# Kernel optimization log

Measured on AMD Instinct MI355X. Metric: run time of the kernel, lower is better.

## Reference

```python
import jax, jax.numpy as jnp
import numpy as np

B, T, E = 4, 2048, 512
H, D = 8, 64            # num_heads, head_size = E // H
HID = H * E             # FFN hidden = num_heads * n_embed (per source)
EPS = 1e-5


def layer_norm(x, g, b):
    mu = jnp.mean(x, axis=-1, keepdims=True)
    var = jnp.var(x, axis=-1, keepdims=True)
    return (x - mu) * jax.lax.rsqrt(var + EPS) * g + b


def setup_inputs() -> dict:
    key = jax.random.key(0)
    ks = jax.random.split(key, 12)
    s_e = 1.0 / np.sqrt(E)
    s_hd = 1.0 / np.sqrt(H * D)
    s_hid = 1.0 / np.sqrt(HID)
    return {
        "x": jax.random.normal(ks[0], (B, T, E), jnp.float32),
        "Wq": jax.random.normal(ks[1], (H, E, D), jnp.float32) * s_e,
        "Wk": jax.random.normal(ks[2], (H, E, D), jnp.float32) * s_e,
        "Wv": jax.random.normal(ks[3], (H, E, D), jnp.float32) * s_e,
        "Wo": jax.random.normal(ks[4], (H * D, E), jnp.float32) * s_hd,
        "bo": jnp.zeros((E,), jnp.float32),
        "W1": jax.random.normal(ks[5], (E, HID), jnp.float32) * s_e,
        "b1": jnp.zeros((HID,), jnp.float32),
        "W2": jax.random.normal(ks[6], (HID, E), jnp.float32) * s_hid,
        "b2": jnp.zeros((E,), jnp.float32),
        "g1": jnp.ones((E,), jnp.float32),
        "be1": jnp.zeros((E,), jnp.float32),
        "g2": jnp.ones((E,), jnp.float32),
        "be2": jnp.zeros((E,), jnp.float32),
    }


def reference(x, Wq, Wk, Wv, Wo, bo, W1, b1, W2, b2, g1, be1, g2, be2):
    # pre-LN decoder block (layer_norm_first=True path)
    xn = layer_norm(x, g1, be1)

    # multi-head causal attention; NOTE: scale is T**-0.5 per the source code
    q = jnp.einsum('bte,hed->bhtd', xn, Wq)
    k = jnp.einsum('bte,hed->bhtd', xn, Wk)
    v = jnp.einsum('bte,hed->bhtd', xn, Wv)
    scores = jnp.einsum('bhtd,bhsd->bhts', q, k) * (T ** -0.5)
    causal = jnp.tril(jnp.ones((T, T), bool))
    scores = jnp.where(causal, scores, -jnp.inf)
    attn = jax.nn.softmax(scores, axis=-1)
    o = jnp.einsum('bhts,bhsd->bhtd', attn, v)           # [B,H,T,D]
    o = o.transpose(0, 2, 1, 3).reshape(B, T, H * D)      # concat heads
    mha = o @ Wo + bo

    x = xn + mha
    xn2 = layer_norm(x, g2, be2)
    ffn = jax.nn.relu(xn2 @ W1 + b1) @ W2 + b2
    return xn2 + ffn
```

## Files before the change

kernel.cpp:

```cpp
#include <hip/hip_runtime.h>
#include <hip/hip_bf16.h>
#include <math.h>

#define Bsz 4
#define Tt 2048
#define Ee 512
#define Hh 8
#define Dd 64
#define HIDs 4096
#define Mrows (Bsz * Tt)

typedef __attribute__((ext_vector_type(8))) short short8;
typedef __attribute__((ext_vector_type(4))) float f32x4;
typedef __attribute__((ext_vector_type(16))) float f32x16;

#define AS1 __attribute__((address_space(1)))
#define AS3 __attribute__((address_space(3)))

__device__ __forceinline__ unsigned short f2bfu(float f) {
    unsigned u = __float_as_uint(f);
    return (unsigned short)((u + 0x7fffu + ((u >> 16) & 1u)) >> 16);
}
__device__ __forceinline__ unsigned short truncbf(float f) {
    return (unsigned short)(__float_as_uint(f) >> 16);
}

__device__ __forceinline__ short8 ld_sw(const __hip_bfloat16* base, int R, int sl) {
    return *(const short8*)(base + R * 32 + (((sl) ^ ((R >> 1) & 3)) << 3));
}

__device__ __forceinline__ void ln_body(const float* __restrict__ x,
        const float* __restrict__ g, const float* __restrict__ b,
        const float* __restrict__ addb,
        float* __restrict__ out_f, __hip_bfloat16* __restrict__ out_bf,
        int row) {
    int tid = threadIdx.x;
    const float* xr = x + (size_t)row * Ee;
    float v0 = xr[tid];
    float v1 = xr[tid + 256];
    float s = v0 + v1;
    float sq = v0 * v0 + v1 * v1;
#pragma unroll
    for (int off = 32; off > 0; off >>= 1) {
        s  += __shfl_xor(s, off, 64);
        sq += __shfl_xor(sq, off, 64);
    }
    __shared__ float ls[4], lq[4];
    int wid = tid >> 6, lane = tid & 63;
    if (lane == 0) { ls[wid] = s; lq[wid] = sq; }
    __syncthreads();
    s  = ls[0] + ls[1] + ls[2] + ls[3];
    sq = lq[0] + lq[1] + lq[2] + lq[3];
    float mean = s * (1.0f / Ee);
    float var  = sq * (1.0f / Ee) - mean * mean;
    float rstd = rsqrtf(var + 1e-5f);
    float o0 = (v0 - mean) * rstd * g[tid]       + b[tid];
    float o1 = (v1 - mean) * rstd * g[tid + 256] + b[tid + 256];
    float* orow = out_f + (size_t)row * Ee;
    orow[tid]       = o0 + addb[tid];
    orow[tid + 256] = o1 + addb[tid + 256];
    __hip_bfloat16* brow = out_bf + (size_t)row * Ee;
    brow[tid]       = __float2bfloat16(o0);
    brow[tid + 256] = __float2bfloat16(o1);
}

__global__ __launch_bounds__(256) void ln_kernel(const float* __restrict__ x,
        const float* __restrict__ g, const float* __restrict__ b,
        const float* __restrict__ addb,
        float* __restrict__ out_f, __hip_bfloat16* __restrict__ out_bf) {
    ln_body(x, g, b, addb, out_f, out_bf, blockIdx.x);
}

__device__ __forceinline__ void tr_tile(const float* __restrict__ in,
        __hip_bfloat16* __restrict__ outp, int R, int C, int c0, int r0) {
    __shared__ float tile[64][65];
    int tc = threadIdx.x & 63, tg = threadIdx.x >> 6;
#pragma unroll
    for (int i = 0; i < 16; ++i) {
        int r = tg * 16 + i;
        tile[r][tc] = in[(size_t)(r0 + r) * C + c0 + tc];
    }
    __syncthreads();
#pragma unroll
    for (int i = 0; i < 16; ++i) {
        int cc = tg * 16 + i;
        outp[(size_t)(c0 + cc) * R + r0 + tc] = __float2bfloat16(tile[tc][cc]);
    }
}
__global__ __launch_bounds__(256) void startup_kernel(
        const float* __restrict__ x, const float* __restrict__ g1,
        const float* __restrict__ be1, const float* __restrict__ bo,
        float* __restrict__ xn, __hip_bfloat16* __restrict__ xn_bf,
        const float* __restrict__ Wq, const float* __restrict__ Wk,
        const float* __restrict__ Wv, const float* __restrict__ Wo,
        const float* __restrict__ W1, const float* __restrict__ W2,
        __hip_bfloat16* __restrict__ bqT, __hip_bfloat16* __restrict__ woT,
        __hip_bfloat16* __restrict__ w1T, __hip_bfloat16* __restrict__ w2T) {
    if (blockIdx.x < Mrows) {
        ln_body(x, g1, be1, bo, xn, xn_bf, blockIdx.x);
        return;
    }
    int blk = blockIdx.x - Mrows;
    if (blk < 192) {
        int p = blk >> 6, h = (blk >> 3) & 7, et = blk & 7;
        const float* W = (p == 0) ? Wq : ((p == 1) ? Wk : Wv);
        float sc = (p == 0) ? 0.022097086912079608f * 1.4426950408889634f : 1.0f;
        __shared__ float tile[64][65];
        int td = threadIdx.x & 63, tg = threadIdx.x >> 6;
#pragma unroll
        for (int i = 0; i < 16; ++i) {
            int e = tg * 16 + i;
            tile[e][td] = W[((size_t)h * Ee + et * 64 + e) * Dd + td] * sc;
        }
        __syncthreads();
#pragma unroll
        for (int i = 0; i < 16; ++i) {
            int d = tg * 16 + i;
            bqT[((size_t)(p * 512 + h * 64 + d)) * Ee + et * 64 + td] =
                __float2bfloat16(tile[td][d]);
        }
    } else if (blk < 256) {
        int t = blk - 192;
        tr_tile(Wo, woT, 512, 512, (t & 7) * 64, (t >> 3) * 64);
    } else if (blk < 768) {
        int t = blk - 256;
        tr_tile(W1, w1T, 512, HIDs, (t & 63) * 64, (t >> 6) * 64);
    } else {
        int t = blk - 768;
        tr_tile(W2, w2T, HIDs, 512, (t & 7) * 64, (t >> 3) * 64);
    }
}

__global__ __launch_bounds__(256) void mfma_gemm(
        const __hip_bfloat16* __restrict__ A, int lda,
        const __hip_bfloat16* __restrict__ B, int ldb,
        __hip_bfloat16* __restrict__ Cb, int ldc, int K, int nx) {
    __shared__ __hip_bfloat16 S[32768];
    int tid = threadIdx.x;
    int lane = tid & 63, wave = tid >> 6;
    int wm = wave >> 1, wn = wave & 1;
    int L = blockIdx.x;
    int slots = (int)gridDim.x >> 3;
    int v = (L & 7) * slots + (L >> 3);
    int bx = v % nx, by = v / nx;
    int row0 = by * 128, col0 = bx * 128;
    f32x4 acc[4][4];
#pragma unroll
    for (int i = 0; i < 4; ++i)
#pragma unroll
        for (int j = 0; j < 4; ++j) acc[i][j] = (f32x4){0.f, 0.f, 0.f, 0.f};

    int fr = lane & 15, sl = lane >> 4;
    int T = K >> 6;

#define STAGEQ(tt, bb)                                                        \
    do {                                                                      \
        int kk_ = (tt) * 64;                                                  \
        _Pragma("unroll")                                                     \
        for (int j = 0; j < 4; ++j) {                                         \
            int c = j * 256 + tid;                                            \
            int p = c >> 9, cp = c & 511;                                     \
            int r = cp >> 2, s = cp & 3;                                      \
            int kg = ((s ^ ((r >> 1) & 3)) << 3);                             \
            int cb = j * 256 + wave * 64;                                     \
            int ko = kk_ + p * 32 + kg;                                       \
            __builtin_amdgcn_global_load_lds(                                 \
                (const AS1 void*)(A + (size_t)(row0 + r) * lda + ko),         \
                (AS3 void*)(S + (bb) * 16384 + cb * 8), 16, 0, 0);            \
            __builtin_amdgcn_global_load_lds(                                 \
                (const AS1 void*)(B + (size_t)(col0 + r) * ldb + ko),         \
                (AS3 void*)(S + (bb) * 16384 + 8192 + cb * 8), 16, 0, 0);     \
        }                                                                     \
    } while (0)

    STAGEQ(0, 0);
    for (int t = 0; t < T; ++t) {
        int tn = (t + 1 < T) ? t + 1 : 0;
        STAGEQ(tn, (t + 1) & 1);
        asm volatile("s_waitcnt vmcnt(8)" ::: "memory");
        __builtin_amdgcn_s_barrier();
        asm volatile("" ::: "memory");
        const __hip_bfloat16* Ab = S + (t & 1) * 16384;
        const __hip_bfloat16* Bb = Ab + 8192;
#pragma unroll
        for (int ks = 0; ks < 2; ++ks) {
            short8 afr[4], bfr[4];
#pragma unroll
            for (int i = 0; i < 4; ++i) {
                afr[i] = ld_sw(Ab + ks * 4096, wm * 64 + i * 16 + fr, sl);
                bfr[i] = ld_sw(Bb + ks * 4096, wn * 64 + i * 16 + fr, sl);
            }
#pragma unroll
            for (int i = 0; i < 4; ++i)
#pragma unroll
                for (int j = 0; j < 4; ++j)
                    acc[i][j] = __builtin_amdgcn_mfma_f32_16x16x32_bf16(afr[i], bfr[j], acc[i][j], 0, 0, 0);
        }
        asm volatile("" ::: "memory");
        __builtin_amdgcn_s_barrier();
        asm volatile("" ::: "memory");
    }
#undef STAGEQ
    asm volatile("s_waitcnt vmcnt(0)" ::: "memory");
    __syncthreads();
    unsigned short* Ew = (unsigned short*)S + wave * 1152;
    const __hip_bfloat16* Er = (const __hip_bfloat16*)Ew;
    int rq = (lane >> 4) << 2;
    int rr = lane >> 2, cb2 = (lane & 3) * 16;
#pragma unroll
    for (int i = 0; i < 4; ++i) {
#pragma unroll
        for (int j = 0; j < 4; ++j)
#pragma unroll
            for (int gi = 0; gi < 4; ++gi)
                Ew[(rq + gi) * 72 + j * 16 + fr] = f2bfu(acc[i][j][gi]);
        uint4 v0 = *(const uint4*)(Er + rr * 72 + cb2);
        uint4 v1 = *(const uint4*)(Er + rr * 72 + cb2 + 8);
        size_t rg = (size_t)(row0 + wm * 64 + i * 16 + rr) * ldc + col0 + wn * 64 + cb2;
        *(uint4*)(Cb + rg)     = v0;
        *(uint4*)(Cb + rg + 8) = v1;
    }
}

__global__ __launch_bounds__(256) void mfma_gemm_n64(
        const __hip_bfloat16* __restrict__ A, int lda,
        const __hip_bfloat16* __restrict__ B, int ldb,
        float* __restrict__ Cf, int ldc, int K, int nx) {
    __shared__ __hip_bfloat16 S[36864];
    int tid = threadIdx.x;
    int lane = tid & 63, wave = tid >> 6;
    int L = blockIdx.x;
    int slots = (int)gridDim.x >> 3;
    int v = (L & 7) * slots + (L >> 3);
    int bx = v % nx, by = v / nx;
    int row0 = by * 128, col0 = bx * 64;
    f32x4 acc[2][4];
#pragma unroll
    for (int i = 0; i < 2; ++i)
#pragma unroll
        for (int j = 0; j < 4; ++j) acc[i][j] = (f32x4){0.f, 0.f, 0.f, 0.f};

    int fr = lane & 15, sl = lane >> 4;
    int T = K >> 6;

#define STAGEN(tt, bb)                                                        \
    do {                                                                      \
        int kk_ = (tt) * 64;                                                  \
        _Pragma("unroll")                                                     \
        for (int j = 0; j < 4; ++j) {                                         \
            int c = j * 256 + tid;                                            \
            int p = c >> 9, cp = c & 511;                                     \
            int r = cp >> 2, s = cp & 3;                                      \
            int kg = ((s ^ ((r >> 1) & 3)) << 3);                             \
            int cb = j * 256 + wave * 64;                                     \
            __builtin_amdgcn_global_load_lds(                                 \
                (const AS1 void*)(A + (size_t)(row0 + r) * lda + kk_ + p * 32 + kg), \
                (AS3 void*)(S + (bb) * 12288 + cb * 8), 16, 0, 0);            \
        }                                                                     \
        _Pragma("unroll")                                                     \
        for (int j = 0; j < 2; ++j) {                                         \
            int c = j * 256 + tid;                                            \
            int p = c >> 8, cp = c & 255;                                     \
            int r = cp >> 2, s = cp & 3;                                      \
            int kg = ((s ^ ((r >> 1) & 3)) << 3);                             \
            int cb = j * 256 + wave * 64;                                     \
            __builtin_amdgcn_global_load_lds(                                 \
                (const AS1 void*)(B + (size_t)(col0 + r) * ldb + kk_ + p * 32 + kg), \
                (AS3 void*)(S + (bb) * 12288 + 8192 + cb * 8), 16, 0, 0);     \
        }                                                                     \
    } while (0)

    STAGEN(0, 0);
    STAGEN(1, 1);
    for (int t = 0; t < T; ++t) {
        int tn = (t + 2 < T) ? t + 2 : 0;
        STAGEN(tn, (t + 2) % 3);
        asm volatile("s_waitcnt vmcnt(12)" ::: "memory");
        __builtin_amdgcn_s_barrier();
        asm volatile("" ::: "memory");
        const __hip_bfloat16* Ab = S + (t % 3) * 12288;
        const __hip_bfloat16* Bb = Ab + 8192;
#pragma unroll
        for (int ks = 0; ks < 2; ++ks) {
            short8 afr[2], bfr[4];
#pragma unroll
            for (int i = 0; i < 2; ++i)
                afr[i] = ld_sw(Ab + ks * 4096, wave * 32 + i * 16 + fr, sl);
#pragma unroll
            for (int j = 0; j < 4; ++j)
                bfr[j] = ld_sw(Bb + ks * 2048, j * 16 + fr, sl);
#pragma unroll
            for (int i = 0; i < 2; ++i)
#pragma unroll
                for (int j = 0; j < 4; ++j)
                    acc[i][j] = __builtin_amdgcn_mfma_f32_16x16x32_bf16(afr[i], bfr[j], acc[i][j], 0, 0, 0);
        }
        asm volatile("" ::: "memory");
        __builtin_amdgcn_s_barrier();
        asm volatile("" ::: "memory");
    }
#undef STAGEN
    asm volatile("s_waitcnt vmcnt(0)" ::: "memory");
    int rq = (lane >> 4) << 2;
#pragma unroll
    for (int i = 0; i < 2; ++i)
#pragma unroll
        for (int j = 0; j < 4; ++j)
#pragma unroll
            for (int gidx = 0; gidx < 4; ++gidx) {
                int r = row0 + wave * 32 + i * 16 + rq + gidx;
                int c = col0 + j * 16 + fr;
                Cf[(size_t)r * ldc + c] += acc[i][j][gidx];
            }
}

__device__ __forceinline__ short8 ld_frag(const __hip_bfloat16* base, int r, int slot) {
    return *(const short8*)(base + r * 64 + ((slot ^ (r & 7)) << 3));
}

__global__ __launch_bounds__(512, 2) void gemm256_8ph(
        const __hip_bfloat16* __restrict__ A, int lda,
        const __hip_bfloat16* __restrict__ B, int ldb,
        __hip_bfloat16* __restrict__ Cb, int ldc, int K,
        const float* __restrict__ bias, int nx) {
    __shared__ __hip_bfloat16 S[65536];
    __hip_bfloat16* Asb = S;
    __hip_bfloat16* Bsb = S + 32768;
    int tid = threadIdx.x;
    int lane = tid & 63, wave = tid >> 6;
    int wm = wave >> 2, wn = wave & 3;
    int fr = lane & 15, l5 = lane >> 4;
    int L = blockIdx.x;
    int slots = (int)gridDim.x >> 3;
    int v = (L & 7) * slots + (L >> 3);
    int bx = v % nx, by = v / nx;
    int row0 = by * 256, col0 = bx * 256;
    int T = K >> 6;

    f32x4 acc[8][4];
#pragma unroll
    for (int i = 0; i < 8; ++i)
#pragma unroll
        for (int j = 0; j < 4; ++j) acc[i][j] = (f32x4){0.f, 0.f, 0.f, 0.f};

#define STAGE_A(tt, hh, bb)                                                   \
    do {                                                                      \
        _Pragma("unroll")                                                     \
        for (int j = 0; j < 2; ++j) {                                         \
            int c = j * 512 + tid;                                            \
            int r = c >> 3;                                                   \
            int sl = (c & 7) ^ (r & 7);                                       \
            int cb = j * 512 + wave * 64;                                     \
            int grow = row0 + ((r >> 6) << 7) + (hh) * 64 + (r & 63);         \
            __builtin_amdgcn_global_load_lds(                                 \
                (const AS1 void*)(A + (size_t)grow * lda + (tt) * 64 + sl * 8), \
                (AS3 void*)(Asb + (bb) * 16384 + (hh) * 8192 + cb * 8), 16, 0, 0); \
        }                                                                     \
    } while (0)
#define STAGE_B(tt, hh, bb)                                                   \
    do {                                                                      \
        _Pragma("unroll")                                                     \
        for (int j = 0; j < 2; ++j) {                                         \
            int c = j * 512 + tid;                                            \
            int r = c >> 3;                                                   \
            int sl = (c & 7) ^ (r & 7);                                       \
            int cb = j * 512 + wave * 64;                                     \
            int gcol = col0 + ((r >> 5) << 6) + (hh) * 32 + (r & 31);         \
            __builtin_amdgcn_global_load_lds(                                 \
                (const AS1 void*)(B + (size_t)gcol * ldb + (tt) * 64 + sl * 8), \
                (AS3 void*)(Bsb + (bb) * 16384 + (hh) * 8192 + cb * 8), 16, 0, 0); \
        }                                                                     \
    } while (0)

    STAGE_A(0, 0, 0);
    STAGE_B(0, 0, 0);
    STAGE_B(0, 1, 0);
    STAGE_A(0, 1, 0);

    short8 a[4][2], b[2][2][2];
    for (int t = 0; t < T; ++t) {
        int buf = t & 1, nb = buf ^ 1;
        int tn = (t + 1 < T) ? t + 1 : 0;
        const __hip_bfloat16* Ab0 = Asb + buf * 16384;
        const __hip_bfloat16* Ab1 = Ab0 + 8192;
        const __hip_bfloat16* Bb0 = Bsb + buf * 16384;
        const __hip_bfloat16* Bb1 = Bb0 + 8192;

        STAGE_A(tn, 0, nb);
        asm volatile("s_waitcnt vmcnt(6)" ::: "memory");
        __builtin_amdgcn_s_barrier();
        asm volatile("" ::: "memory");
#pragma unroll
        for (int i = 0; i < 4; ++i)
#pragma unroll
            for (int ks = 0; ks < 2; ++ks)
                a[i][ks] = ld_frag(Ab0, wm * 64 + i * 16 + fr, ks * 4 + l5);
#pragma unroll
        for (int jj = 0; jj < 2; ++jj)
#pragma unroll
            for (int ks = 0; ks < 2; ++ks)
                b[0][jj][ks] = ld_frag(Bb0, wn * 32 + jj * 16 + fr, ks * 4 + l5);
        __builtin_amdgcn_s_setprio(1);
#pragma unroll
        for (int i = 0; i < 4; ++i)
#pragma unroll
            for (int jj = 0; jj < 2; ++jj)
#pragma unroll
                for (int ks = 0; ks < 2; ++ks)
                    acc[i][jj] = __builtin_amdgcn_mfma_f32_16x16x32_bf16(
                        a[i][ks], b[0][jj][ks], acc[i][jj], 0, 0, 0);
        __builtin_amdgcn_s_setprio(0);
        asm volatile("" ::: "memory");
        __builtin_amdgcn_s_barrier();
        asm volatile("" ::: "memory");

        STAGE_B(tn, 0, nb);
        asm volatile("s_waitcnt vmcnt(6)" ::: "memory");
        __builtin_amdgcn_s_barrier();
        asm volatile("" ::: "memory");
#pragma unroll
        for (int jj = 0; jj < 2; ++jj)
#pragma unroll
            for (int ks = 0; ks < 2; ++ks)
                b[1][jj][ks] = ld_frag(Bb1, wn * 32 + jj * 16 + fr, ks * 4 + l5);
        __builtin_amdgcn_s_setprio(1);
#pragma unroll
        for (int i = 0; i < 4; ++i)
#pragma unroll
            for (int jj = 0; jj < 2; ++jj)
#pragma unroll
                for (int ks = 0; ks < 2; ++ks)
                    acc[i][2 + jj] = __builtin_amdgcn_mfma_f32_16x16x32_bf16(
                        a[i][ks], b[1][jj][ks], acc[i][2 + jj], 0, 0, 0);
        __builtin_amdgcn_s_setprio(0);
        asm volatile("" ::: "memory");
        __builtin_amdgcn_s_barrier();
        asm volatile("" ::: "memory");

        STAGE_B(tn, 1, nb);
        asm volatile("s_waitcnt vmcnt(6)" ::: "memory");
        __builtin_amdgcn_s_barrier();
        asm volatile("" ::: "memory");
#pragma unroll
        for (int i = 0; i < 4; ++i)
#pragma unroll
            for (int ks = 0; ks < 2; ++ks)
                a[i][ks] = ld_frag(Ab1, wm * 64 + i * 16 + fr, ks * 4 + l5);
        __builtin_amdgcn_s_setprio(1);
#pragma unroll
        for (int i = 0; i < 4; ++i)
#pragma unroll
            for (int jj = 0; jj < 2; ++jj)
#pragma unroll
                for (int ks = 0; ks < 2; ++ks)
                    acc[4 + i][2 + jj] = __builtin_amdgcn_mfma_f32_16x16x32_bf16(
                        a[i][ks], b[1][jj][ks], acc[4 + i][2 + jj], 0, 0, 0);
        __builtin_amdgcn_s_setprio(0);
        asm volatile("" ::: "memory");
        __builtin_amdgcn_s_barrier();
        asm volatile("" ::: "memory");

        STAGE_A(tn, 1, nb);
        asm volatile("" ::: "memory");
        __builtin_amdgcn_s_barrier();
        asm volatile("" ::: "memory");
        __builtin_amdgcn_s_setprio(1);
#pragma unroll
        for (int i = 0; i < 4; ++i)
#pragma unroll
            for (int jj = 0; jj < 2; ++jj)
#pragma unroll
                for (int ks = 0; ks < 2; ++ks)
                    acc[4 + i][jj] = __builtin_amdgcn_mfma_f32_16x16x32_bf16(
                        a[i][ks], b[0][jj][ks], acc[4 + i][jj], 0, 0, 0);
        __builtin_amdgcn_s_setprio(0);
        asm volatile("" ::: "memory");
        __builtin_amdgcn_s_barrier();
        asm volatile("" ::: "memory");
    }
#undef STAGE_A
#undef STAGE_B

    __syncthreads();
    float bvv[4];
#pragma unroll
    for (int nj = 0; nj < 4; ++nj) bvv[nj] = bias[col0 + wn * 64 + nj * 16 + fr];
    unsigned short* Ew = (unsigned short*)S + wave * 1152;
    const __hip_bfloat16* Er = (const __hip_bfloat16*)Ew;
    int rq = l5 << 2;
    int rr = lane >> 2, cb2 = (lane & 3) * 16;
#pragma unroll
    for (int mi = 0; mi < 8; ++mi) {
#pragma unroll
        for (int nj = 0; nj < 4; ++nj)
#pragma unroll
            for (int gi = 0; gi < 4; ++gi) {
                float tv = acc[mi][nj][gi] + bvv[nj];
                Ew[(rq + gi) * 72 + nj * 16 + fr] = f2bfu(tv > 0.f ? tv : 0.f);
            }
        uint4 v0 = *(const uint4*)(Er + rr * 72 + cb2);
        uint4 v1 = *(const uint4*)(Er + rr * 72 + cb2 + 8);
        size_t rg = (size_t)(row0 + wm * 128 + mi * 16 + rr) * ldc
                    + col0 + wn * 64 + cb2;
        *(uint4*)(Cb + rg)     = v0;
        *(uint4*)(Cb + rg + 8) = v1;
    }
}

__global__ __launch_bounds__(256) void attn_mfma(const __hip_bfloat16* __restrict__ qkvb,
        __hip_bfloat16* __restrict__ ob) {
    __shared__ __hip_bfloat16 KsS[2][64 * 72];
    __shared__ __hip_bfloat16 VtS[2][64 * 72];
    __shared__ __hip_bfloat16 PsS[4 * 32 * 72];
    __hip_bfloat16* Qs = PsS;

    const unsigned short* q16 = (const unsigned short*)qkvb;
    int tid  = threadIdx.x;
    int lane = tid & 63, wave = tid >> 6;
    int l31 = lane & 31, l5 = lane >> 5;
    int blk = blockIdx.x;
    int qb  = 15 - (blk >> 5);
    int bh  = blk & 31;
    int b = bh >> 3, h = bh & 7;
    int base = qb * 128;
    size_t tokbase = (size_t)b * Tt;
    int qoff = h * 64, koff = 512 + h * 64, voff = 1024 + h * 64;

    {
        int q = tid >> 1, dg = (tid & 1) * 32;
        const unsigned short* src = q16 + (tokbase + base + q) * 1536 + qoff + dg;
        uint4 a  = *(const uint4*)src;
        uint4 b4 = *(const uint4*)(src + 8);
        uint4 c4 = *(const uint4*)(src + 16);
        uint4 d4 = *(const uint4*)(src + 24);
        *(uint4*)(Qs + q * 72 + dg)      = a;
        *(uint4*)(Qs + q * 72 + dg + 8)  = b4;
        *(uint4*)(Qs + q * 72 + dg + 16) = c4;
        *(uint4*)(Qs + q * 72 + dg + 24) = d4;
    }
    __syncthreads();
    short8 aq[4];
#pragma unroll
    for (int kd = 0; kd < 4; ++kd)
        aq[kd] = *(const short8*)(Qs + (wave * 32 + l31) * 72 + kd * 16 + l5 * 8);

    short8 ones;
#pragma unroll
    for (int i = 0; i < 8; ++i) ones[i] = (short)0x3F80;

    f32x16 acc[2], accL;
#pragma unroll
    for (int i = 0; i < 16; ++i) { acc[0][i] = 0.f; acc[1][i] = 0.f; accL[i] = 0.f; }
    __hip_bfloat16* Psw = PsS + wave * (32 * 72);
    unsigned short* Psw16 = (unsigned short*)Psw;

    int s_k = tid >> 2, dg_k = (tid & 3) * 16;
    int sp = (tid & 31) * 2, dg8 = (tid >> 5) * 8;
    uint4 kr0, kr1, va, vb;
    {
        const unsigned short* kp = q16 + (tokbase + s_k) * 1536 + koff + dg_k;
        kr0 = *(const uint4*)kp;
        kr1 = *(const uint4*)(kp + 8);
        const unsigned short* vp = q16 + (tokbase + sp) * 1536 + voff + dg8;
        va = *(const uint4*)vp;
        vb = *(const uint4*)(vp + 1536);
    }

    int tmax = 2 * qb + 1;
    for (int tile = 0; tile <= tmax; ++tile) {
        int buf = tile & 1;
        *(uint4*)(KsS[buf] + s_k * 72 + dg_k)     = kr0;
        *(uint4*)(KsS[buf] + s_k * 72 + dg_k + 8) = kr1;
        {
            unsigned a0[4] = {va.x, va.y, va.z, va.w};
            unsigned b0[4] = {vb.x, vb.y, vb.z, vb.w};
#pragma unroll
            for (int i = 0; i < 4; ++i) {
                unsigned p0 = (a0[i] & 0xffffu) | (b0[i] << 16);
                unsigned p1 = (a0[i] >> 16) | (b0[i] & 0xffff0000u);
                *(unsigned*)(VtS[buf] + (dg8 + 2 * i) * 72 + sp)     = p0;
                *(unsigned*)(VtS[buf] + (dg8 + 2 * i + 1) * 72 + sp) = p1;
            }
        }
        __syncthreads();
        if (tile < tmax) {
            int s1 = (tile + 1) * 64;
            const unsigned short* kp = q16 + (tokbase + s1 + s_k) * 1536 + koff + dg_k;
            kr0 = *(const uint4*)kp;
            kr1 = *(const uint4*)(kp + 8);
            const unsigned short* vp = q16 + (tokbase + s1 + sp) * 1536 + voff + dg8;
            va = *(const uint4*)vp;
            vb = *(const uint4*)(vp + 1536);
        }
        if (tile == tmax && wave < 2) continue;
        f32x16 Sc[2];
#pragma unroll
        for (int i = 0; i < 16; ++i) { Sc[0][i] = 0.f; Sc[1][i] = 0.f; }
#pragma unroll
        for (int st = 0; st < 2; ++st)
#pragma unroll
            for (int kd = 0; kd < 4; ++kd) {
                short8 bk = *(const short8*)(KsS[buf] + (st * 32 + l31) * 72 + kd * 16 + l5 * 8);
                Sc[st] = __builtin_amdgcn_mfma_f32_32x32x16_bf16(aq[kd], bk, Sc[st], 0, 0, 0);
            }
        if (tile >= 2 * qb) {
            int s0t = tile * 64;
            int qrb = base + wave * 32 + 4 * l5;
#pragma unroll
            for (int st = 0; st < 2; ++st) {
                int sg = s0t + st * 32 + l31;
#pragma unroll
                for (int reg = 0; reg < 16; ++reg) {
                    int qr = qrb + (reg & 3) + 8 * (reg >> 2);
                    if (sg > qr) Sc[st][reg] = -1e30f;
                }
            }
        }
#pragma unroll
        for (int st = 0; st < 2; ++st)
#pragma unroll
            for (int reg = 0; reg < 16; ++reg) {
                int pr = (reg & 3) + 8 * (reg >> 2) + 4 * l5;
                Psw16[pr * 72 + st * 32 + l31] =
                    truncbf(__builtin_amdgcn_exp2f(Sc[st][reg]));
            }
#pragma unroll
        for (int ks = 0; ks < 4; ++ks) {
            short8 ap = *(const short8*)(Psw + l31 * 72 + ks * 16 + l5 * 8);
            accL = __builtin_amdgcn_mfma_f32_32x32x16_bf16(ap, ones, accL, 0, 0, 0);
#pragma unroll
            for (int dt = 0; dt < 2; ++dt) {
                short8 bv = *(const short8*)(VtS[buf] + (dt * 32 + l31) * 72 + ks * 16 + l5 * 8);
                acc[dt] = __builtin_amdgcn_mfma_f32_32x32x16_bf16(ap, bv, acc[dt], 0, 0, 0);
            }
        }
    }
#pragma unroll
    for (int reg = 0; reg < 16; ++reg) {
        float rl = 1.0f / accL[reg];
        int qr = base + wave * 32 + (reg & 3) + 8 * (reg >> 2) + 4 * l5;
#pragma unroll
        for (int dt = 0; dt < 2; ++dt)
            ob[(tokbase + qr) * 512 + h * 64 + dt * 32 + l31] =
                __float2bfloat16(acc[dt][reg] * rl);
    }
}

extern "C" void kernel_launch(void* const* d_in, const int* in_sizes, int n_in,
                              void* d_out, int out_size, void* d_ws, size_t ws_size,
                              hipStream_t stream) {
    const float* x   = (const float*)d_in[0];
    const float* Wq  = (const float*)d_in[1];
    const float* Wk  = (const float*)d_in[2];
    const float* Wv  = (const float*)d_in[3];
    const float* Wo  = (const float*)d_in[4];
    const float* bo  = (const float*)d_in[5];
    const float* W1  = (const float*)d_in[6];
    const float* b1  = (const float*)d_in[7];
    const float* W2  = (const float*)d_in[8];
    const float* b2  = (const float*)d_in[9];
    const float* g1  = (const float*)d_in[10];
    const float* be1 = (const float*)d_in[11];
    const float* g2  = (const float*)d_in[12];
    const float* be2 = (const float*)d_in[13];
    float* out = (float*)d_out;

    char* ws = (char*)d_ws;
    __hip_bfloat16* bqT    = (__hip_bfloat16*)(ws);
    __hip_bfloat16* woT    = (__hip_bfloat16*)(ws + 1572864);
    __hip_bfloat16* w1T    = (__hip_bfloat16*)(ws + 2097152);
    __hip_bfloat16* w2T    = (__hip_bfloat16*)(ws + 6291456);
    float*          xn     = (float*)(ws + 10485760);
    __hip_bfloat16* xn_bf  = (__hip_bfloat16*)(ws + 27262976);
    __hip_bfloat16* qkv_bf = (__hip_bfloat16*)(ws + 35651584);
    __hip_bfloat16* o_bf   = (__hip_bfloat16*)(ws + 60817408);
    __hip_bfloat16* h_bf   = (__hip_bfloat16*)(ws + 35651584);

    startup_kernel<<<Mrows + 1280, 256, 0, stream>>>(
        x, g1, be1, bo, xn, xn_bf, Wq, Wk, Wv, Wo, W1, W2, bqT, woT, w1T, w2T);
    mfma_gemm<<<768, 256, 0, stream>>>(
        xn_bf, 512, bqT, 512, qkv_bf, 1536, 512, 12);
    attn_mfma<<<Bsz * Hh * (Tt / 128), 256, 0, stream>>>(qkv_bf, o_bf);
    mfma_gemm_n64<<<512, 256, 0, stream>>>(
        o_bf, 512, woT, 512, xn, 512, 512, 8);
    ln_kernel<<<Mrows, 256, 0, stream>>>(xn, g2, be2, b2, out, xn_bf);
    gemm256_8ph<<<512, 512, 0, stream>>>(
        xn_bf, 512, w1T, 512, h_bf, HIDs, 512, b1, 16);
    mfma_gemm_n64<<<512, 256, 0, stream>>>(
        h_bf, HIDs, w2T, HIDs, out, 512, HIDs, 8);
}
```

Before: 301.1 us.

## Replace FFN down-projection GEMM with 256x256 split-K kernel using atomic accumulation

The second FFN GEMM (K=4096, N=512) moves from a 64-wide-N kernel on 512 blocks to a 256x256-tile 8-phase kernel that splits K into four chunks of 1024, with 256 blocks each atomically adding fp32 partials into the output. The main loop of the existing 256-tile kernel is pulled into a macro so both kernels share it. The aim is more reuse per loaded tile and fewer redundant A/B loads than the narrow-N kernel. In exchange it adds atomic-add traffic and nondeterministic summation order, and it relies on the output already holding the residual and bias from the layer-norm kernel.

```diff
diff --git a/kernel.cpp b/kernel.cpp
--- a/kernel.cpp
+++ b/kernel.cpp
@@ -372,114 +372,110 @@
         }                                                                     \
     } while (0)
 
-    STAGE_A(0, 0, 0);
-    STAGE_B(0, 0, 0);
-    STAGE_B(0, 1, 0);
-    STAGE_A(0, 1, 0);
-
-    short8 a[4][2], b[2][2][2];
-    for (int t = 0; t < T; ++t) {
-        int buf = t & 1, nb = buf ^ 1;
-        int tn = (t + 1 < T) ? t + 1 : 0;
-        const __hip_bfloat16* Ab0 = Asb + buf * 16384;
-        const __hip_bfloat16* Ab1 = Ab0 + 8192;
-        const __hip_bfloat16* Bb0 = Bsb + buf * 16384;
-        const __hip_bfloat16* Bb1 = Bb0 + 8192;
-
-        STAGE_A(tn, 0, nb);
-        asm volatile("s_waitcnt vmcnt(6)" ::: "memory");
-        __builtin_amdgcn_s_barrier();
-        asm volatile("" ::: "memory");
-#pragma unroll
-        for (int i = 0; i < 4; ++i)
-#pragma unroll
-            for (int ks = 0; ks < 2; ++ks)
-                a[i][ks] = ld_frag(Ab0, wm * 64 + i * 16 + fr, ks * 4 + l5);
-#pragma unroll
-        for (int jj = 0; jj < 2; ++jj)
-#pragma unroll
-            for (int ks = 0; ks < 2; ++ks)
-                b[0][jj][ks] = ld_frag(Bb0, wn * 32 + jj * 16 + fr, ks * 4 + l5);
-        __builtin_amdgcn_s_setprio(1);
-#pragma unroll
-        for (int i = 0; i < 4; ++i)
-#pragma unroll
-            for (int jj = 0; jj < 2; ++jj)
-#pragma unroll
-                for (int ks = 0; ks < 2; ++ks)
-                    acc[i][jj] = __builtin_amdgcn_mfma_f32_16x16x32_bf16(
-                        a[i][ks], b[0][jj][ks], acc[i][jj], 0, 0, 0);
-        __builtin_amdgcn_s_setprio(0);
-        asm volatile("" ::: "memory");
-        __builtin_amdgcn_s_barrier();
-        asm volatile("" ::: "memory");
-
-        STAGE_B(tn, 0, nb);
-        asm volatile("s_waitcnt vmcnt(6)" ::: "memory");
-        __builtin_amdgcn_s_barrier();
-        asm volatile("" ::: "memory");
-#pragma unroll
-        for (int jj = 0; jj < 2; ++jj)
-#pragma unroll
-            for (int ks = 0; ks < 2; ++ks)
-                b[1][jj][ks] = ld_frag(Bb1, wn * 32 + jj * 16 + fr, ks * 4 + l5);
-        __builtin_amdgcn_s_setprio(1);
-#pragma unroll
-        for (int i = 0; i < 4; ++i)
-#pragma unroll
-            for (int jj = 0; jj < 2; ++jj)
-#pragma unroll
-                for (int ks = 0; ks < 2; ++ks)
-                    acc[i][2 + jj] = __builtin_amdgcn_mfma_f32_16x16x32_bf16(
-                        a[i][ks], b[1][jj][ks], acc[i][2 + jj], 0, 0, 0);
-        __builtin_amdgcn_s_setprio(0);
-        asm volatile("" ::: "memory");
-        __builtin_amdgcn_s_barrier();
-        asm volatile("" ::: "memory");
-
-        STAGE_B(tn, 1, nb);
-        asm volatile("s_waitcnt vmcnt(6)" ::: "memory");
-        __builtin_amdgcn_s_barrier();
-        asm volatile("" ::: "memory");
-#pragma unroll
-        for (int i = 0; i < 4; ++i)
-#pragma unroll
-            for (int ks = 0; ks < 2; ++ks)
-                a[i][ks] = ld_frag(Ab1, wm * 64 + i * 16 + fr, ks * 4 + l5);
-        __builtin_amdgcn_s_setprio(1);
-#pragma unroll
-        for (int i = 0; i < 4; ++i)
-#pragma unroll
-            for (int jj = 0; jj < 2; ++jj)
-#pragma unroll
-                for (int ks = 0; ks < 2; ++ks)
-                    acc[4 + i][2 + jj] = __builtin_amdgcn_mfma_f32_16x16x32_bf16(
-                        a[i][ks], b[1][jj][ks], acc[4 + i][2 + jj], 0, 0, 0);
-        __builtin_amdgcn_s_setprio(0);
-        asm volatile("" ::: "memory");
-        __builtin_amdgcn_s_barrier();
-        asm volatile("" ::: "memory");
-
-        STAGE_A(tn, 1, nb);
-        asm volatile("" ::: "memory");
-        __builtin_amdgcn_s_barrier();
-        asm volatile("" ::: "memory");
-        __builtin_amdgcn_s_setprio(1);
-#pragma unroll
-        for (int i = 0; i < 4; ++i)
-#pragma unroll
-            for (int jj = 0; jj < 2; ++jj)
-#pragma unroll
-                for (int ks = 0; ks < 2; ++ks)
-                    acc[4 + i][jj] = __builtin_amdgcn_mfma_f32_16x16x32_bf16(
-                        a[i][ks], b[0][jj][ks], acc[4 + i][jj], 0, 0, 0);
-        __builtin_amdgcn_s_setprio(0);
-        asm volatile("" ::: "memory");
-        __builtin_amdgcn_s_barrier();
-        asm volatile("" ::: "memory");
-    }
-#undef STAGE_A
-#undef STAGE_B
+#define KLOOP_8PH                                                             \
+    STAGE_A(0, 0, 0);                                                         \
+    STAGE_B(0, 0, 0);                                                         \
+    STAGE_B(0, 1, 0);                                                         \
+    STAGE_A(0, 1, 0);                                                         \
+    short8 a[4][2], b[2][2][2];                                               \
+    for (int t = 0; t < T; ++t) {                                             \
+        int buf = t & 1, nb = buf ^ 1;                                        \
+        int tn = (t + 1 < T) ? t + 1 : 0;                                     \
+        const __hip_bfloat16* Ab0 = Asb + buf * 16384;                        \
+        const __hip_bfloat16* Ab1 = Ab0 + 8192;                               \
+        const __hip_bfloat16* Bb0 = Bsb + buf * 16384;                        \
+        const __hip_bfloat16* Bb1 = Bb0 + 8192;                               \
+        STAGE_A(tn, 0, nb);                                                   \
+        asm volatile("s_waitcnt vmcnt(6)" ::: "memory");                      \
+        __builtin_amdgcn_s_barrier();                                         \
+        asm volatile("" ::: "memory");                                        \
+        _Pragma("unroll")                                                     \
+        for (int i = 0; i < 4; ++i)                                           \
+            _Pragma("unroll")                                                 \
+            for (int ks = 0; ks < 2; ++ks)                                    \
+                a[i][ks] = ld_frag(Ab0, wm * 64 + i * 16 + fr, ks * 4 + l5);  \
+        _Pragma("unroll")                                                     \
+        for (int jj = 0; jj < 2; ++jj)                                        \
+            _Pragma("unroll")                                                 \
+            for (int ks = 0; ks < 2; ++ks)                                    \
+                b[0][jj][ks] = ld_frag(Bb0, wn * 32 + jj * 16 + fr, ks * 4 + l5); \
+        __builtin_amdgcn_s_setprio(1);                                        \
+        _Pragma("unroll")                                                     \
+        for (int i = 0; i < 4; ++i)                                           \
+            _Pragma("unroll")                                                 \
+            for (int jj = 0; jj < 2; ++jj)                                    \
+                _Pragma("unroll")                                             \
+                for (int ks = 0; ks < 2; ++ks)                                \
+                    acc[i][jj] = __builtin_amdgcn_mfma_f32_16x16x32_bf16(     \
+                        a[i][ks], b[0][jj][ks], acc[i][jj], 0, 0, 0);         \
+        __builtin_amdgcn_s_setprio(0);                                        \
+        asm volatile("" ::: "memory");                                        \
+        __builtin_amdgcn_s_barrier();                                         \
+        asm volatile("" ::: "memory");                                        \
+        STAGE_B(tn, 0, nb);                                                   \
+        asm volatile("s_waitcnt vmcnt(6)" ::: "memory");                      \
+        __builtin_amdgcn_s_barrier();                                         \
+        asm volatile("" ::: "memory");                                        \
+        _Pragma("unroll")                                                     \
+        for (int jj = 0; jj < 2; ++jj)                                        \
+            _Pragma("unroll")                                                 \
+            for (int ks = 0; ks < 2; ++ks)                                    \
+                b[1][jj][ks] = ld_frag(Bb1, wn * 32 + jj * 16 + fr, ks * 4 + l5); \
+        __builtin_amdgcn_s_setprio(1);                                        \
+        _Pragma("unroll")                                                     \
+        for (int i = 0; i < 4; ++i)                                           \
+            _Pragma("unroll")                                                 \
+            for (int jj = 0; jj < 2; ++jj)                                    \
+                _Pragma("unroll")                                             \
+                for (int ks = 0; ks < 2; ++ks)                                \
+                    acc[i][2 + jj] = __builtin_amdgcn_mfma_f32_16x16x32_bf16( \
+                        a[i][ks], b[1][jj][ks], acc[i][2 + jj], 0, 0, 0);     \
+        __builtin_amdgcn_s_setprio(0);                                        \
+        asm volatile("" ::: "memory");                                        \
+        __builtin_amdgcn_s_barrier();                                         \
+        asm volatile("" ::: "memory");                                        \
+        STAGE_B(tn, 1, nb);                                                   \
+        asm volatile("s_waitcnt vmcnt(6)" ::: "memory");                      \
+        __builtin_amdgcn_s_barrier();                                         \
+        asm volatile("" ::: "memory");                                        \
+        _Pragma("unroll")                                                     \
+        for (int i = 0; i < 4; ++i)                                           \
+            _Pragma("unroll")                                                 \
+            for (int ks = 0; ks < 2; ++ks)                                    \
+                a[i][ks] = ld_frag(Ab1, wm * 64 + i * 16 + fr, ks * 4 + l5);  \
+        __builtin_amdgcn_s_setprio(1);                                        \
+        _Pragma("unroll")                                                     \
+        for (int i = 0; i < 4; ++i)                                           \
+            _Pragma("unroll")                                                 \
+            for (int jj = 0; jj < 2; ++jj)                                    \
+                _Pragma("unroll")                                             \
+                for (int ks = 0; ks < 2; ++ks)                                \
+                    acc[4 + i][2 + jj] = __builtin_amdgcn_mfma_f32_16x16x32_bf16( \
+                        a[i][ks], b[1][jj][ks], acc[4 + i][2 + jj], 0, 0, 0); \
+        __builtin_amdgcn_s_setprio(0);                                        \
+        asm volatile("" ::: "memory");                                        \
+        __builtin_amdgcn_s_barrier();                                         \
+        asm volatile("" ::: "memory");                                        \
+        STAGE_A(tn, 1, nb);                                                   \
+        asm volatile("" ::: "memory");                                        \
+        __builtin_amdgcn_s_barrier();                                         \
+        asm volatile("" ::: "memory");                                        \
+        __builtin_amdgcn_s_setprio(1);                                        \
+        _Pragma("unroll")                                                     \
+        for (int i = 0; i < 4; ++i)                                           \
+            _Pragma("unroll")                                                 \
+            for (int jj = 0; jj < 2; ++jj)                                    \
+                _Pragma("unroll")                                             \
+                for (int ks = 0; ks < 2; ++ks)                                \
+                    acc[4 + i][jj] = __builtin_amdgcn_mfma_f32_16x16x32_bf16( \
+                        a[i][ks], b[0][jj][ks], acc[4 + i][jj], 0, 0, 0);     \
+        __builtin_amdgcn_s_setprio(0);                                        \
+        asm volatile("" ::: "memory");                                        \
+        __builtin_amdgcn_s_barrier();                                         \
+        asm volatile("" ::: "memory");                                        \
+    }
+
+    KLOOP_8PH
 
     __syncthreads();
     float bvv[4];
@@ -505,6 +501,54 @@
         *(uint4*)(Cb + rg)     = v0;
         *(uint4*)(Cb + rg + 8) = v1;
     }
+}
+
+__global__ __launch_bounds__(512, 2) void gemm256_splitk(
+        const __hip_bfloat16* __restrict__ A, int lda,
+        const __hip_bfloat16* __restrict__ B, int ldb,
+        float* __restrict__ Cf, int ldc, int Ksp, int nx) {
+    __shared__ __hip_bfloat16 S[65536];
+    __hip_bfloat16* Asb = S;
+    __hip_bfloat16* Bsb = S + 32768;
+    int tid = threadIdx.x;
+    int lane = tid & 63, wave = tid >> 6;
+    int wm = wave >> 2, wn = wave & 3;
+    int fr = lane & 15, l5 = lane >> 4;
+    int L = blockIdx.x;
+    int slots = (int)gridDim.x >> 3;
+    int v = (L & 7) * slots + (L >> 3);
+    int bx = v % nx;
+    int kq = (v / nx) & 3;
+    int by = v / (nx * 4);
+    int row0 = by * 256, col0 = bx * 256;
+    A += (size_t)kq * Ksp;
+    B += (size_t)kq * Ksp;
+    int T = Ksp >> 6;
+
+    f32x4 acc[8][4];
+#pragma unroll
+    for (int i = 0; i < 8; ++i)
+#pragma unroll
+        for (int j = 0; j < 4; ++j) acc[i][j] = (f32x4){0.f, 0.f, 0.f, 0.f};
+
+    KLOOP_8PH
+
+#undef STAGE_A
+#undef STAGE_B
+#undef KLOOP_8PH
+
+    asm volatile("s_waitcnt vmcnt(0)" ::: "memory");
+    int rq = l5 << 2;
+#pragma unroll
+    for (int mi = 0; mi < 8; ++mi)
+#pragma unroll
+        for (int nj = 0; nj < 4; ++nj)
+#pragma unroll
+            for (int gi = 0; gi < 4; ++gi) {
+                int r = row0 + wm * 128 + mi * 16 + rq + gi;
+                int c = col0 + wn * 64 + nj * 16 + fr;
+                unsafeAtomicAdd(&Cf[(size_t)r * ldc + c], acc[mi][nj][gi]);
+            }
 }
 
 __global__ __launch_bounds__(256) void attn_mfma(const __hip_bfloat16* __restrict__ qkvb,
@@ -686,6 +730,6 @@
     ln_kernel<<<Mrows, 256, 0, stream>>>(xn, g2, be2, b2, out, xn_bf);
     gemm256_8ph<<<512, 512, 0, stream>>>(
         xn_bf, 512, w1T, 512, h_bf, HIDs, 512, b1, 16);
-    mfma_gemm_n64<<<512, 256, 0, stream>>>(
-        h_bf, HIDs, w2T, HIDs, out, 512, HIDs, 8);
-}
+    gemm256_splitk<<<256, 512, 0, stream>>>(
+        h_bf, HIDs, w2T, HIDs, out, 512, 1024, 2);
+}
```

Measured after the change: 321.0 us. 6.6% more time.

## Use split-K 128x128 tile kernel with atomic accumulation for FFN down-projection

Applied to the files above, without the earlier changes.

Replaces the 128x64-tile GEMM for the second FFN matmul (K=4096) with a new kernel using 128x128 tiles and a 2-way split over K. Each half accumulates into the output with atomic float adds, relying on out already holding the residual and bias. This raises per-block data reuse while keeping 512 blocks in flight. The cost is twice the atomic traffic on the output, and the summation order becomes non-deterministic.

```diff
diff --git a/kernel.cpp b/kernel.cpp
--- a/kernel.cpp
+++ b/kernel.cpp
@@ -220,6 +220,94 @@
         *(uint4*)(Cb + rg)     = v0;
         *(uint4*)(Cb + rg + 8) = v1;
     }
+}
+
+__global__ __launch_bounds__(256) void mfma_gemm_sk(
+        const __hip_bfloat16* __restrict__ A, int lda,
+        const __hip_bfloat16* __restrict__ B, int ldb,
+        float* __restrict__ Cf, int ldc, int Ksp, int nx) {
+    __shared__ __hip_bfloat16 S[32768];
+    int tid = threadIdx.x;
+    int lane = tid & 63, wave = tid >> 6;
+    int wm = wave >> 1, wn = wave & 1;
+    int L = blockIdx.x;
+    int slots = (int)gridDim.x >> 3;
+    int v = (L & 7) * slots + (L >> 3);
+    int kq = v & 1;
+    int u = v >> 1;
+    int bx = u % nx, by = u / nx;
+    int row0 = by * 128, col0 = bx * 128;
+    A += (size_t)kq * Ksp;
+    B += (size_t)kq * Ksp;
+    f32x4 acc[4][4];
+#pragma unroll
+    for (int i = 0; i < 4; ++i)
+#pragma unroll
+        for (int j = 0; j < 4; ++j) acc[i][j] = (f32x4){0.f, 0.f, 0.f, 0.f};
+
+    int fr = lane & 15, sl = lane >> 4;
+    int T = Ksp >> 6;
+
+#define STAGES(tt, bb)                                                        \
+    do {                                                                      \
+        int kk_ = (tt) * 64;                                                  \
+        _Pragma("unroll")                                                     \
+        for (int j = 0; j < 4; ++j) {                                         \
+            int c = j * 256 + tid;                                            \
+            int p = c >> 9, cp = c & 511;                                     \
+            int r = cp >> 2, s = cp & 3;                                      \
+            int kg = ((s ^ ((r >> 1) & 3)) << 3);                             \
+            int cb = j * 256 + wave * 64;                                     \
+            int ko = kk_ + p * 32 + kg;                                       \
+            __builtin_amdgcn_global_load_lds(                                 \
+                (const AS1 void*)(A + (size_t)(row0 + r) * lda + ko),         \
+                (AS3 void*)(S + (bb) * 16384 + cb * 8), 16, 0, 0);            \
+            __builtin_amdgcn_global_load_lds(                                 \
+                (const AS1 void*)(B + (size_t)(col0 + r) * ldb + ko),         \
+                (AS3 void*)(S + (bb) * 16384 + 8192 + cb * 8), 16, 0, 0);     \
+        }                                                                     \
+    } while (0)
+
+    STAGES(0, 0);
+    for (int t = 0; t < T; ++t) {
+        int tn = (t + 1 < T) ? t + 1 : 0;
+        STAGES(tn, (t + 1) & 1);
+        asm volatile("s_waitcnt vmcnt(8)" ::: "memory");
+        __builtin_amdgcn_s_barrier();
+        asm volatile("" ::: "memory");
+        const __hip_bfloat16* Ab = S + (t & 1) * 16384;
+        const __hip_bfloat16* Bb = Ab + 8192;
+#pragma unroll
+        for (int ks = 0; ks < 2; ++ks) {
+            short8 afr[4], bfr[4];
+#pragma unroll
+            for (int i = 0; i < 4; ++i) {
+                afr[i] = ld_sw(Ab + ks * 4096, wm * 64 + i * 16 + fr, sl);
+                bfr[i] = ld_sw(Bb + ks * 4096, wn * 64 + i * 16 + fr, sl);
+            }
+#pragma unroll
+            for (int i = 0; i < 4; ++i)
+#pragma unroll
+                for (int j = 0; j < 4; ++j)
+                    acc[i][j] = __builtin_amdgcn_mfma_f32_16x16x32_bf16(afr[i], bfr[j], acc[i][j], 0, 0, 0);
+        }
+        asm volatile("" ::: "memory");
+        __builtin_amdgcn_s_barrier();
+        asm volatile("" ::: "memory");
+    }
+#undef STAGES
+    asm volatile("s_waitcnt vmcnt(0)" ::: "memory");
+    int rq = (lane >> 4) << 2;
+#pragma unroll
+    for (int i = 0; i < 4; ++i)
+#pragma unroll
+        for (int j = 0; j < 4; ++j)
+#pragma unroll
+            for (int gi = 0; gi < 4; ++gi) {
+                int r = row0 + wm * 64 + i * 16 + rq + gi;
+                int c = col0 + wn * 64 + j * 16 + fr;
+                unsafeAtomicAdd(&Cf[(size_t)r * ldc + c], acc[i][j][gi]);
+            }
 }
 
 __global__ __launch_bounds__(256) void mfma_gemm_n64(
@@ -686,6 +774,6 @@
     ln_kernel<<<Mrows, 256, 0, stream>>>(xn, g2, be2, b2, out, xn_bf);
     gemm256_8ph<<<512, 512, 0, stream>>>(
         xn_bf, 512, w1T, 512, h_bf, HIDs, 512, b1, 16);
-    mfma_gemm_n64<<<512, 256, 0, stream>>>(
-        h_bf, HIDs, w2T, HIDs, out, 512, HIDs, 8);
-}
+    mfma_gemm_sk<<<512, 256, 0, stream>>>(
+        h_bf, HIDs, w2T, HIDs, out, 512, 2048, 4);
+}
```

Result: no change. 297.1 us (-1.3%).

## Replace 256x256 eight-phase FFN1 GEMM with simpler 128x128 tiled kernel

Applied to the files above, without the earlier changes.

The FFN up-projection GEMM (8192x4096, K=512) moves from a 256x256-tile, 512-thread kernel with an eight-phase interleaved load/compute schedule to a 128x128-tile, 256-thread kernel with a plain double-buffered K loop. The grid grows from 512 to 2048 blocks and shared memory per block halves, which should raise occupancy and balance work across CUs for this short K. In exchange, each tile has lower arithmetic intensity, so more global and LDS traffic per FLOP, and the fine-grained phase overlap is lost. It reuses the existing swizzled fragment loader and the bias+ReLU bf16 epilogue.

```diff
diff --git a/kernel.cpp b/kernel.cpp
--- a/kernel.cpp
+++ b/kernel.cpp
@@ -214,6 +214,103 @@
 #pragma unroll
             for (int gi = 0; gi < 4; ++gi)
                 Ew[(rq + gi) * 72 + j * 16 + fr] = f2bfu(acc[i][j][gi]);
+        uint4 v0 = *(const uint4*)(Er + rr * 72 + cb2);
+        uint4 v1 = *(const uint4*)(Er + rr * 72 + cb2 + 8);
+        size_t rg = (size_t)(row0 + wm * 64 + i * 16 + rr) * ldc + col0 + wn * 64 + cb2;
+        *(uint4*)(Cb + rg)     = v0;
+        *(uint4*)(Cb + rg + 8) = v1;
+    }
+}
+
+__global__ __launch_bounds__(256) void gemm128_ffn1(
+        const __hip_bfloat16* __restrict__ A, int lda,
+        const __hip_bfloat16* __restrict__ B, int ldb,
+        __hip_bfloat16* __restrict__ Cb, int ldc, int K,
+        const float* __restrict__ bias, int nx) {
+    __shared__ __hip_bfloat16 S[32768];
+    int tid = threadIdx.x;
+    int lane = tid & 63, wave = tid >> 6;
+    int wm = wave >> 1, wn = wave & 1;
+    int L = blockIdx.x;
+    int slots = (int)gridDim.x >> 3;
+    int v = (L & 7) * slots + (L >> 3);
+    int bx = v % nx, by = v / nx;
+    int row0 = by * 128, col0 = bx * 128;
+    f32x4 acc[4][4];
+#pragma unroll
+    for (int i = 0; i < 4; ++i)
+#pragma unroll
+        for (int j = 0; j < 4; ++j) acc[i][j] = (f32x4){0.f, 0.f, 0.f, 0.f};
+
+    int fr = lane & 15, sl = lane >> 4;
+    int T = K >> 6;
+
+#define STAGEF(tt, bb)                                                        \
+    do {                                                                      \
+        int kk_ = (tt) * 64;                                                  \
+        _Pragma("unroll")                                                     \
+        for (int j = 0; j < 4; ++j) {                                         \
+            int c = j * 256 + tid;                                            \
+            int p = c >> 9, cp = c & 511;                                     \
+            int r = cp >> 2, s = cp & 3;                                      \
+            int kg = ((s ^ ((r >> 1) & 3)) << 3);                             \
+            int cb = j * 256 + wave * 64;                                     \
+            int ko = kk_ + p * 32 + kg;                                       \
+            __builtin_amdgcn_global_load_lds(                                 \
+                (const AS1 void*)(A + (size_t)(row0 + r) * lda + ko),         \
+                (AS3 void*)(S + (bb) * 16384 + cb * 8), 16, 0, 0);            \
+            __builtin_amdgcn_global_load_lds(                                 \
+                (const AS1 void*)(B + (size_t)(col0 + r) * ldb + ko),         \
+                (AS3 void*)(S + (bb) * 16384 + 8192 + cb * 8), 16, 0, 0);     \
+        }                                                                     \
+    } while (0)
+
+    STAGEF(0, 0);
+    for (int t = 0; t < T; ++t) {
+        int tn = (t + 1 < T) ? t + 1 : 0;
+        STAGEF(tn, (t + 1) & 1);
+        asm volatile("s_waitcnt vmcnt(8)" ::: "memory");
+        __builtin_amdgcn_s_barrier();
+        asm volatile("" ::: "memory");
+        const __hip_bfloat16* Ab = S + (t & 1) * 16384;
+        const __hip_bfloat16* Bb = Ab + 8192;
+#pragma unroll
+        for (int ks = 0; ks < 2; ++ks) {
+            short8 afr[4], bfr[4];
+#pragma unroll
+            for (int i = 0; i < 4; ++i) {
+                afr[i] = ld_sw(Ab + ks * 4096, wm * 64 + i * 16 + fr, sl);
+                bfr[i] = ld_sw(Bb + ks * 4096, wn * 64 + i * 16 + fr, sl);
+            }
+#pragma unroll
+            for (int i = 0; i < 4; ++i)
+#pragma unroll
+                for (int j = 0; j < 4; ++j)
+                    acc[i][j] = __builtin_amdgcn_mfma_f32_16x16x32_bf16(afr[i], bfr[j], acc[i][j], 0, 0, 0);
+        }
+        asm volatile("" ::: "memory");
+        __builtin_amdgcn_s_barrier();
+        asm volatile("" ::: "memory");
+    }
+#undef STAGEF
+    asm volatile("s_waitcnt vmcnt(0)" ::: "memory");
+    __syncthreads();
+    float bv[4];
+#pragma unroll
+    for (int j = 0; j < 4; ++j) bv[j] = bias[col0 + wn * 64 + j * 16 + fr];
+    unsigned short* Ew = (unsigned short*)S + wave * 1152;
+    const __hip_bfloat16* Er = (const __hip_bfloat16*)Ew;
+    int rq = (lane >> 4) << 2;
+    int rr = lane >> 2, cb2 = (lane & 3) * 16;
+#pragma unroll
+    for (int i = 0; i < 4; ++i) {
+#pragma unroll
+        for (int j = 0; j < 4; ++j)
+#pragma unroll
+            for (int gi = 0; gi < 4; ++gi) {
+                float tv = acc[i][j][gi] + bv[j];
+                Ew[(rq + gi) * 72 + j * 16 + fr] = f2bfu(tv > 0.f ? tv : 0.f);
+            }
         uint4 v0 = *(const uint4*)(Er + rr * 72 + cb2);
         uint4 v1 = *(const uint4*)(Er + rr * 72 + cb2 + 8);
         size_t rg = (size_t)(row0 + wm * 64 + i * 16 + rr) * ldc + col0 + wn * 64 + cb2;
@@ -314,199 +411,6 @@
             }
 }
 
-__device__ __forceinline__ short8 ld_frag(const __hip_bfloat16* base, int r, int slot) {
-    return *(const short8*)(base + r * 64 + ((slot ^ (r & 7)) << 3));
-}
-
-__global__ __launch_bounds__(512, 2) void gemm256_8ph(
-        const __hip_bfloat16* __restrict__ A, int lda,
-        const __hip_bfloat16* __restrict__ B, int ldb,
-        __hip_bfloat16* __restrict__ Cb, int ldc, int K,
-        const float* __restrict__ bias, int nx) {
-    __shared__ __hip_bfloat16 S[65536];
-    __hip_bfloat16* Asb = S;
-    __hip_bfloat16* Bsb = S + 32768;
-    int tid = threadIdx.x;
-    int lane = tid & 63, wave = tid >> 6;
-    int wm = wave >> 2, wn = wave & 3;
-    int fr = lane & 15, l5 = lane >> 4;
-    int L = blockIdx.x;
-    int slots = (int)gridDim.x >> 3;
-    int v = (L & 7) * slots + (L >> 3);
-    int bx = v % nx, by = v / nx;
-    int row0 = by * 256, col0 = bx * 256;
-    int T = K >> 6;
-
-    f32x4 acc[8][4];
-#pragma unroll
-    for (int i = 0; i < 8; ++i)
-#pragma unroll
-        for (int j = 0; j < 4; ++j) acc[i][j] = (f32x4){0.f, 0.f, 0.f, 0.f};
-
-#define STAGE_A(tt, hh, bb)                                                   \
-    do {                                                                      \
-        _Pragma("unroll")                                                     \
-        for (int j = 0; j < 2; ++j) {                                         \
-            int c = j * 512 + tid;                                            \
-            int r = c >> 3;                                                   \
-            int sl = (c & 7) ^ (r & 7);                                       \
-            int cb = j * 512 + wave * 64;                                     \
-            int grow = row0 + ((r >> 6) << 7) + (hh) * 64 + (r & 63);         \
-            __builtin_amdgcn_global_load_lds(                                 \
-                (const AS1 void*)(A + (size_t)grow * lda + (tt) * 64 + sl * 8), \
-                (AS3 void*)(Asb + (bb) * 16384 + (hh) * 8192 + cb * 8), 16, 0, 0); \
-        }                                                                     \
-    } while (0)
-#define STAGE_B(tt, hh, bb)                                                   \
-    do {                                                                      \
-        _Pragma("unroll")                                                     \
-        for (int j = 0; j < 2; ++j) {                                         \
-            int c = j * 512 + tid;                                            \
-            int r = c >> 3;                                                   \
-            int sl = (c & 7) ^ (r & 7);                                       \
-            int cb = j * 512 + wave * 64;                                     \
-            int gcol = col0 + ((r >> 5) << 6) + (hh) * 32 + (r & 31);         \
-            __builtin_amdgcn_global_load_lds(                                 \
-                (const AS1 void*)(B + (size_t)gcol * ldb + (tt) * 64 + sl * 8), \
-                (AS3 void*)(Bsb + (bb) * 16384 + (hh) * 8192 + cb * 8), 16, 0, 0); \
-        }                                                                     \
-    } while (0)
-
-    STAGE_A(0, 0, 0);
-    STAGE_B(0, 0, 0);
-    STAGE_B(0, 1, 0);
-    STAGE_A(0, 1, 0);
-
-    short8 a[4][2], b[2][2][2];
-    for (int t = 0; t < T; ++t) {
-        int buf = t & 1, nb = buf ^ 1;
-        int tn = (t + 1 < T) ? t + 1 : 0;
-        const __hip_bfloat16* Ab0 = Asb + buf * 16384;
-        const __hip_bfloat16* Ab1 = Ab0 + 8192;
-        const __hip_bfloat16* Bb0 = Bsb + buf * 16384;
-        const __hip_bfloat16* Bb1 = Bb0 + 8192;
-
-        STAGE_A(tn, 0, nb);
-        asm volatile("s_waitcnt vmcnt(6)" ::: "memory");
-        __builtin_amdgcn_s_barrier();
-        asm volatile("" ::: "memory");
-#pragma unroll
-        for (int i = 0; i < 4; ++i)
-#pragma unroll
-            for (int ks = 0; ks < 2; ++ks)
-                a[i][ks] = ld_frag(Ab0, wm * 64 + i * 16 + fr, ks * 4 + l5);
-#pragma unroll
-        for (int jj = 0; jj < 2; ++jj)
-#pragma unroll
-            for (int ks = 0; ks < 2; ++ks)
-                b[0][jj][ks] = ld_frag(Bb0, wn * 32 + jj * 16 + fr, ks * 4 + l5);
-        __builtin_amdgcn_s_setprio(1);
-#pragma unroll
-        for (int i = 0; i < 4; ++i)
-#pragma unroll
-            for (int jj = 0; jj < 2; ++jj)
-#pragma unroll
-                for (int ks = 0; ks < 2; ++ks)
-                    acc[i][jj] = __builtin_amdgcn_mfma_f32_16x16x32_bf16(
-                        a[i][ks], b[0][jj][ks], acc[i][jj], 0, 0, 0);
-        __builtin_amdgcn_s_setprio(0);
-        asm volatile("" ::: "memory");
-        __builtin_amdgcn_s_barrier();
-        asm volatile("" ::: "memory");
-
-        STAGE_B(tn, 0, nb);
-        asm volatile("s_waitcnt vmcnt(6)" ::: "memory");
-        __builtin_amdgcn_s_barrier();
-        asm volatile("" ::: "memory");
-#pragma unroll
-        for (int jj = 0; jj < 2; ++jj)
-#pragma unroll
-            for (int ks = 0; ks < 2; ++ks)
-                b[1][jj][ks] = ld_frag(Bb1, wn * 32 + jj * 16 + fr, ks * 4 + l5);
-        __builtin_amdgcn_s_setprio(1);
-#pragma unroll
-        for (int i = 0; i < 4; ++i)
-#pragma unroll
-            for (int jj = 0; jj < 2; ++jj)
-#pragma unroll
-                for (int ks = 0; ks < 2; ++ks)
-                    acc[i][2 + jj] = __builtin_amdgcn_mfma_f32_16x16x32_bf16(
-                        a[i][ks], b[1][jj][ks], acc[i][2 + jj], 0, 0, 0);
-        __builtin_amdgcn_s_setprio(0);
-        asm volatile("" ::: "memory");
-        __builtin_amdgcn_s_barrier();
-        asm volatile("" ::: "memory");
-
-        STAGE_B(tn, 1, nb);
-        asm volatile("s_waitcnt vmcnt(6)" ::: "memory");
-        __builtin_amdgcn_s_barrier();
-        asm volatile("" ::: "memory");
-#pragma unroll
-        for (int i = 0; i < 4; ++i)
-#pragma unroll
-            for (int ks = 0; ks < 2; ++ks)
-                a[i][ks] = ld_frag(Ab1, wm * 64 + i * 16 + fr, ks * 4 + l5);
-        __builtin_amdgcn_s_setprio(1);
-#pragma unroll
-        for (int i = 0; i < 4; ++i)
-#pragma unroll
-            for (int jj = 0; jj < 2; ++jj)
-#pragma unroll
-                for (int ks = 0; ks < 2; ++ks)
-                    acc[4 + i][2 + jj] = __builtin_amdgcn_mfma_f32_16x16x32_bf16(
-                        a[i][ks], b[1][jj][ks], acc[4 + i][2 + jj], 0, 0, 0);
-        __builtin_amdgcn_s_setprio(0);
-        asm volatile("" ::: "memory");
-        __builtin_amdgcn_s_barrier();
-        asm volatile("" ::: "memory");
-
-        STAGE_A(tn, 1, nb);
-        asm volatile("" ::: "memory");
-        __builtin_amdgcn_s_barrier();
-        asm volatile("" ::: "memory");
-        __builtin_amdgcn_s_setprio(1);
-#pragma unroll
-        for (int i = 0; i < 4; ++i)
-#pragma unroll
-            for (int jj = 0; jj < 2; ++jj)
-#pragma unroll
-                for (int ks = 0; ks < 2; ++ks)
-                    acc[4 + i][jj] = __builtin_amdgcn_mfma_f32_16x16x32_bf16(
-                        a[i][ks], b[0][jj][ks], acc[4 + i][jj], 0, 0, 0);
-        __builtin_amdgcn_s_setprio(0);
-        asm volatile("" ::: "memory");
-        __builtin_amdgcn_s_barrier();
-        asm volatile("" ::: "memory");
-    }
-#undef STAGE_A
-#undef STAGE_B
-
-    __syncthreads();
-    float bvv[4];
-#pragma unroll
-    for (int nj = 0; nj < 4; ++nj) bvv[nj] = bias[col0 + wn * 64 + nj * 16 + fr];
-    unsigned short* Ew = (unsigned short*)S + wave * 1152;
-    const __hip_bfloat16* Er = (const __hip_bfloat16*)Ew;
-    int rq = l5 << 2;
-    int rr = lane >> 2, cb2 = (lane & 3) * 16;
-#pragma unroll
-    for (int mi = 0; mi < 8; ++mi) {
-#pragma unroll
-        for (int nj = 0; nj < 4; ++nj)
-#pragma unroll
-            for (int gi = 0; gi < 4; ++gi) {
-                float tv = acc[mi][nj][gi] + bvv[nj];
-                Ew[(rq + gi) * 72 + nj * 16 + fr] = f2bfu(tv > 0.f ? tv : 0.f);
-            }
-        uint4 v0 = *(const uint4*)(Er + rr * 72 + cb2);
-        uint4 v1 = *(const uint4*)(Er + rr * 72 + cb2 + 8);
-        size_t rg = (size_t)(row0 + wm * 128 + mi * 16 + rr) * ldc
-                    + col0 + wn * 64 + cb2;
-        *(uint4*)(Cb + rg)     = v0;
-        *(uint4*)(Cb + rg + 8) = v1;
-    }
-}
-
 __global__ __launch_bounds__(256) void attn_mfma(const __hip_bfloat16* __restrict__ qkvb,
         __hip_bfloat16* __restrict__ ob) {
     __shared__ __hip_bfloat16 KsS[2][64 * 72];
@@ -684,8 +588,8 @@
     mfma_gemm_n64<<<512, 256, 0, stream>>>(
         o_bf, 512, woT, 512, xn, 512, 512, 8);
     ln_kernel<<<Mrows, 256, 0, stream>>>(xn, g2, be2, b2, out, xn_bf);
-    gemm256_8ph<<<512, 512, 0, stream>>>(
-        xn_bf, 512, w1T, 512, h_bf, HIDs, 512, b1, 16);
+    gemm128_ffn1<<<2048, 256, 0, stream>>>(
+        xn_bf, 512, w1T, 512, h_bf, HIDs, 512, b1, 32);
     mfma_gemm_n64<<<512, 256, 0, stream>>>(
         h_bf, HIDs, w2T, HIDs, out, 512, HIDs, 8);
 }
```

After: 305.1 us. No clear change (+1.3%).
